# Kernel tuning notes

Measured on AMD Instinct MI355X. Metric: run time of the kernel, lower is better.

## Reference

```python
import jax, jax.numpy as jnp
import numpy as np

C, D, B, NS = 1000, 256, 16384, 200000
MOMENTUM = 0.1
TOPK = 5
EPS = 1e-12  # torch F.normalize default eps


def _cos_distance(a, b):
    # 0.5 * (1 - cos_sim) between rows of a [N,D] and rows of b [M,D]
    a = a / jnp.maximum(jnp.linalg.norm(a, axis=1, keepdims=True), EPS)
    b = b / jnp.maximum(jnp.linalg.norm(b, axis=1, keepdims=True), EPS)
    return 0.5 * (1.0 - jnp.einsum('nd,md->nm', a, b))


def setup_inputs() -> dict:
    key = jax.random.key(0)
    k1, k2, k3, k4 = jax.random.split(key, 4)
    return {
        'feature_source': jax.random.normal(k1, (B, D), jnp.float32),
        'center_mem': jax.random.normal(k2, (C, D), jnp.float32),
        'source_mem': jax.random.normal(k3, (NS, D), jnp.float32),
        'class2center': jnp.zeros((C, 2), jnp.float32),
        'interdist': jnp.zeros((C, C, 2), jnp.float32),
        'label_source': jax.random.randint(k4, (B,), 0, C, jnp.int32),
        'index_source': jnp.arange(B, dtype=jnp.int32),
    }


def reference(feature_source, center_mem, source_mem, class2center, interdist,
              label_source, index_source):
    # --- featuredistance2center: scatter-add per-class count and distance ---
    d1 = _cos_distance(feature_source, center_mem)            # [B, C]
    dist_at_label = jnp.take_along_axis(d1, label_source[:, None], axis=1)[:, 0]  # [B]
    class2center_new = class2center.at[label_source, 0].add(1.0)
    class2center_new = class2center_new.at[label_source, 1].add(dist_at_label)

    # --- update_center (labels_value=None): center += sum of features per class ---
    center_new = center_mem + jax.ops.segment_sum(feature_source, label_source,
                                                  num_segments=C)  # [C, D]

    # --- update_source: momentum scatter update of the source feature bank ---
    old = source_mem[index_source]                             # [B, D]
    source_mem_new = source_mem.at[index_source].set((1.0 - MOMENTUM) * old
                                                     + MOMENTUM * feature_source)

    # --- sourcefeature2differertcenter: topk-smallest distances, scatter-add ---
    d2 = _cos_distance(feature_source, center_new)             # [B, C]
    neg_vals, top_idx = jax.lax.top_k(-d2, TOPK)               # smallest distances
    top_dists = -neg_vals                                      # [B, TOPK]
    top1, top2 = top_idx[:, 0], top_idx[:, 1]
    inter = jnp.abs(top_dists[:, 0] - top_dists[:, 1])         # [B]
    interdist_new = interdist.at[top1, top2, 0].add(1.0)
    interdist_new = interdist_new.at[top1, top2, 1].add(inter)

    return (center_new, source_mem_new, class2center_new, interdist_new)
```

## Files before the change

### kernel.cpp

```cpp
#include <hip/hip_runtime.h>
#include <math.h>

#define Cc 1000
#define Cpad 1024
#define Dd 256
#define Bb 16384
#define NSs 200000
#define MOM 0.1f
#define EPSV 1e-12f
#define EPSC 0.10f

#define OUT_CENTER 0
#define OUT_SRC (Cc*Dd)
#define OUT_C2C (OUT_SRC + (size_t)NSs*Dd)
#define OUT_INTER (OUT_C2C + Cc*2)

#define SCR_SCORES 0
#define SCR_FB ((size_t)Bb * Cpad)
#define SCR_CB (SCR_FB + (size_t)Bb*Dd/2)

#define WS_CHAT 0
#define WS_INVF (Cc*Dd)

#define NEG_BIG (-3.4e38f)

typedef __bf16 bf16x8 __attribute__((ext_vector_type(8)));
typedef float  f32x4  __attribute__((ext_vector_type(4)));

__device__ __forceinline__ ushort f2bf(float f) {
    uint u = __float_as_uint(f);
    u += 0x7FFFu + ((u >> 16) & 1u);
    return (ushort)(u >> 16);
}

__device__ __forceinline__ void upd_top2(float& s1, int& i1, float& s2, int& i2,
                                         float s, int i) {
    if (s > s1 || (s == s1 && i < i1)) {
        s2 = s1; i2 = i1; s1 = s; i1 = i;
    } else if (s > s2 || (s == s2 && i < i2)) {
        s2 = s; i2 = i;
    }
}

__global__ void k_copy(const float4* __restrict__ interdist,
                       const float4* __restrict__ c2c,
                       const float4* __restrict__ cmem,
                       float4* __restrict__ out_inter,
                       float4* __restrict__ out_c2c,
                       float4* __restrict__ out_center) {
    int i = blockIdx.x * blockDim.x + threadIdx.x;
    const int n_inter = Cc * Cc * 2 / 4;
    const int n_c2c   = Cc * 2 / 4;
    const int n_cm    = Cc * Dd / 4;
    if (i < n_inter) {
        out_inter[i] = interdist[i];
    } else if (i < n_inter + n_c2c) {
        out_c2c[i - n_inter] = c2c[i - n_inter];
    } else if (i < n_inter + n_c2c + n_cm) {
        out_center[i - n_inter - n_c2c] = cmem[i - n_inter - n_c2c];
    }
}

__global__ void k_rows_a(const float* __restrict__ feat, const float* __restrict__ cmem,
                         const int* __restrict__ label,
                         float* __restrict__ out_center, float* __restrict__ out_c2c,
                         float* __restrict__ ws_invf, ushort* __restrict__ fb) {
    int wid  = threadIdx.x >> 6;
    int lane = threadIdx.x & 63;
    int row  = blockIdx.x * 4 + wid;
    if (row >= Bb) return;

    const float4 f4 = *(const float4*)(feat + (size_t)row * Dd + lane * 4);
    int lab = label[row];
    const float4 c4 = *(const float4*)(cmem + (size_t)lab * Dd + lane * 4);

    ushort4 h;
    h.x = f2bf(f4.x); h.y = f2bf(f4.y); h.z = f2bf(f4.z); h.w = f2bf(f4.w);
    *(ushort4*)(fb + (size_t)row * Dd + lane * 4) = h;

    float fs = f4.x*f4.x + f4.y*f4.y + f4.z*f4.z + f4.w*f4.w;
    float dt = f4.x*c4.x + f4.y*c4.y + f4.z*c4.z + f4.w*c4.w;
    float cs = c4.x*c4.x + c4.y*c4.y + c4.z*c4.z + c4.w*c4.w;
    #pragma unroll
    for (int off = 32; off; off >>= 1) {
        fs += __shfl_xor(fs, off);
        dt += __shfl_xor(dt, off);
        cs += __shfl_xor(cs, off);
    }
    float invf = 1.0f / fmaxf(sqrtf(fs), EPSV);
    if (lane == 0) {
        ws_invf[row] = invf;
        float invc = 1.0f / fmaxf(sqrtf(cs), EPSV);
        float d1 = 0.5f * (1.0f - dt * invf * invc);
        atomicAdd(out_c2c + lab * 2,     1.0f);
        atomicAdd(out_c2c + lab * 2 + 1, d1);
    }
    atomicAdd(out_center + (size_t)lab * Dd + lane * 4 + 0, f4.x);
    atomicAdd(out_center + (size_t)lab * Dd + lane * 4 + 1, f4.y);
    atomicAdd(out_center + (size_t)lab * Dd + lane * 4 + 2, f4.z);
    atomicAdd(out_center + (size_t)lab * Dd + lane * 4 + 3, f4.w);
}

__global__ void k_chat(const float* __restrict__ out_center, float* __restrict__ chat,
                       ushort* __restrict__ cb) {
    int c = blockIdx.x;
    int lane = threadIdx.x;
    if (c >= Cc) {
        ushort4 z; z.x = 0; z.y = 0; z.z = 0; z.w = 0;
        *(ushort4*)(cb + (size_t)c * Dd + lane * 4) = z;
        return;
    }
    float4 v = *(const float4*)(out_center + (size_t)c * Dd + lane * 4);
    float ss = v.x*v.x + v.y*v.y + v.z*v.z + v.w*v.w;
    #pragma unroll
    for (int off = 32; off; off >>= 1) ss += __shfl_xor(ss, off);
    float inv = 1.0f / fmaxf(sqrtf(ss), EPSV);
    float4 r; r.x = v.x*inv; r.y = v.y*inv; r.z = v.z*inv; r.w = v.w*inv;
    *(float4*)(chat + (size_t)c * Dd + lane * 4) = r;
    ushort4 h;
    h.x = f2bf(r.x); h.y = f2bf(r.y); h.z = f2bf(r.z); h.w = f2bf(r.w);
    *(ushort4*)(cb + (size_t)c * Dd + lane * 4) = h;
}

__global__ __launch_bounds__(256) void k_gemm(const ushort* __restrict__ fb,
                                              const ushort* __restrict__ cb,
                                              float* __restrict__ scores) {
    int wid  = threadIdx.x >> 6;
    int lane = threadIdx.x & 63;
    int rl = lane & 15;
    int kg = lane >> 4;
    int row0 = blockIdx.y * 64;
    int c0   = blockIdx.x * 256 + wid * 64;

    const ushort* fp = fb + (size_t)(row0 + rl) * Dd + kg * 8;
    const ushort* cp = cb + (size_t)(c0  + rl) * Dd + kg * 8;

    f32x4 acc[4][4];
    f32x4 z = {0.f, 0.f, 0.f, 0.f};
    #pragma unroll
    for (int mi = 0; mi < 4; mi++)
        #pragma unroll
        for (int ni = 0; ni < 4; ni++)
            acc[mi][ni] = z;

    #pragma unroll
    for (int ks = 0; ks < 8; ks++) {
        bf16x8 a[4], b[4];
        #pragma unroll
        for (int mi = 0; mi < 4; mi++)
            a[mi] = *(const bf16x8*)(fp + (size_t)mi * 16 * Dd + ks * 32);
        #pragma unroll
        for (int ni = 0; ni < 4; ni++)
            b[ni] = *(const bf16x8*)(cp + (size_t)ni * 16 * Dd + ks * 32);
        #pragma unroll
        for (int mi = 0; mi < 4; mi++)
            #pragma unroll
            for (int ni = 0; ni < 4; ni++)
                acc[mi][ni] = __builtin_amdgcn_mfma_f32_16x16x32_bf16(a[mi], b[ni], acc[mi][ni], 0, 0, 0);
    }

    #pragma unroll
    for (int mi = 0; mi < 4; mi++)
        #pragma unroll
        for (int ni = 0; ni < 4; ni++)
            #pragma unroll
            for (int r = 0; r < 4; r++)
                scores[(size_t)(row0 + mi*16 + kg*4 + r) * Cpad + (c0 + ni*16 + rl)] = acc[mi][ni][r];
}

__global__ __launch_bounds__(256) void k_sel(const float* __restrict__ scores,
                                             const float* __restrict__ feat,
                                             const float* __restrict__ chat,
                                             const float* __restrict__ ws_invf,
                                             float* __restrict__ out_inter) {
    __shared__ int cnt[4];
    __shared__ int clist[4][32];
    int wid  = threadIdx.x >> 6;
    int lane = threadIdx.x & 63;
    int row  = blockIdx.x * 4 + wid;
    if (lane == 0) cnt[wid] = 0;

    const float4* sp = (const float4*)(scores + (size_t)row * Cpad);
    float v[16];
    float s1 = NEG_BIG, s2 = NEG_BIG;
    int   i1 = 0x7fffffff, i2 = 0x7fffffff;
    #pragma unroll
    for (int j = 0; j < 4; j++) {
        float4 q = sp[j * 64 + lane];
        int cbase = j * 256 + lane * 4;
        v[j*4+0] = q.x; v[j*4+1] = q.y; v[j*4+2] = q.z; v[j*4+3] = q.w;
        if (cbase + 0 < Cc) upd_top2(s1, i1, s2, i2, q.x, cbase + 0);
        if (cbase + 1 < Cc) upd_top2(s1, i1, s2, i2, q.y, cbase + 1);
        if (cbase + 2 < Cc) upd_top2(s1, i1, s2, i2, q.z, cbase + 2);
        if (cbase + 3 < Cc) upd_top2(s1, i1, s2, i2, q.w, cbase + 3);
    }
    #pragma unroll
    for (int off = 1; off < 64; off <<= 1) {
        float ps1 = __shfl_xor(s1, off), ps2 = __shfl_xor(s2, off);
        int   pi1 = __shfl_xor(i1, off), pi2 = __shfl_xor(i2, off);
        upd_top2(s1, i1, s2, i2, ps1, pi1);
        upd_top2(s1, i1, s2, i2, ps2, pi2);
    }
    float thr = s2 - EPSC;
    #pragma unroll
    for (int j = 0; j < 16; j++) {
        int c = (j >> 2) * 256 + lane * 4 + (j & 3);
        if (v[j] >= thr && c < Cc) {
            int slot = atomicAdd(&cnt[wid], 1);
            if (slot < 32) clist[wid][slot] = c;
        }
    }
    __syncthreads();
    int n = cnt[wid]; if (n > 32) n = 32;

    const float4 f4 = *(const float4*)(feat + (size_t)row * Dd + lane * 4);
    float S1 = NEG_BIG, S2 = NEG_BIG;
    int   I1 = 0x7fffffff, I2 = 0x7fffffff;
    for (int k = 0; k < n; k++) {
        int c = clist[wid][k];
        const float4 c4 = *(const float4*)(chat + (size_t)c * Dd + lane * 4);
        float d = f4.x*c4.x + f4.y*c4.y + f4.z*c4.z + f4.w*c4.w;
        #pragma unroll
        for (int off = 32; off; off >>= 1) d += __shfl_xor(d, off);
        upd_top2(S1, I1, S2, I2, d, c);
    }
    if (lane == 0) {
        float inter = 0.5f * ws_invf[row] * (S1 - S2);
        size_t off2 = ((size_t)I1 * Cc + I2) * 2;
        atomicAdd(out_inter + off2,     1.0f);
        atomicAdd(out_inter + off2 + 1, inter);
    }
}

__global__ void k_srccopy(const float4* __restrict__ src, float4* __restrict__ dst, int n4) {
    int stride = gridDim.x * blockDim.x;
    for (int i = blockIdx.x * blockDim.x + threadIdx.x; i < n4; i += stride)
        dst[i] = src[i];
}

__global__ void k_rows_b(const float* __restrict__ feat, const float* __restrict__ smem,
                         const int* __restrict__ index, float* __restrict__ out_src) {
    int wid  = threadIdx.x >> 6;
    int lane = threadIdx.x & 63;
    int row  = blockIdx.x * 4 + wid;
    if (row >= Bb) return;
    int idx = index[row];
    const float4 f4 = *(const float4*)(feat + (size_t)row * Dd + lane * 4);
    const float4 o4 = *(const float4*)(smem + (size_t)idx * Dd + lane * 4);
    float4 r;
    r.x = (1.0f - MOM) * o4.x + MOM * f4.x;
    r.y = (1.0f - MOM) * o4.y + MOM * f4.y;
    r.z = (1.0f - MOM) * o4.z + MOM * f4.z;
    r.w = (1.0f - MOM) * o4.w + MOM * f4.w;
    *(float4*)(out_src + (size_t)idx * Dd + lane * 4) = r;
}

extern "C" void kernel_launch(void* const* d_in, const int* in_sizes, int n_in,
                              void* d_out, int out_size, void* d_ws, size_t ws_size,
                              hipStream_t stream) {
    const float* feat   = (const float*)d_in[0];
    const float* cmem   = (const float*)d_in[1];
    const float* smem   = (const float*)d_in[2];
    const float* c2c    = (const float*)d_in[3];
    const float* inter  = (const float*)d_in[4];
    const int*   label  = (const int*)d_in[5];
    const int*   index  = (const int*)d_in[6];

    float* out = (float*)d_out;
    float* out_center = out + OUT_CENTER;
    float* out_src    = out + OUT_SRC;
    float* out_c2c    = out + OUT_C2C;
    float* out_inter  = out + OUT_INTER;

    float* ws    = (float*)d_ws;
    float* chat  = ws + WS_CHAT;
    float* winvf = ws + WS_INVF;

    float*  scores = out_src + SCR_SCORES;
    ushort* fb     = (ushort*)(out_src + SCR_FB);
    ushort* cb     = (ushort*)(out_src + SCR_CB);

    {
        int total4 = Cc*Cc*2/4 + Cc*2/4 + Cc*Dd/4;
        int blocks = (total4 + 255) / 256;
        k_copy<<<blocks, 256, 0, stream>>>((const float4*)inter, (const float4*)c2c,
                                           (const float4*)cmem,
                                           (float4*)out_inter, (float4*)out_c2c,
                                           (float4*)out_center);
    }
    k_rows_a<<<Bb / 4, 256, 0, stream>>>(feat, cmem, label, out_center, out_c2c, winvf, fb);
    k_chat<<<Cpad, 64, 0, stream>>>(out_center, chat, cb);
    {
        dim3 grid(4, Bb / 64);
        k_gemm<<<grid, 256, 0, stream>>>(fb, cb, scores);
    }
    k_sel<<<Bb / 4, 256, 0, stream>>>(scores, feat, chat, winvf, out_inter);
    {
        int n4 = NSs * Dd / 4;
        k_srccopy<<<2048, 256, 0, stream>>>((const float4*)smem, (float4*)out_src, n4);
    }
    k_rows_b<<<Bb / 4, 256, 0, stream>>>(feat, smem, index, out_src);
}
```

Measured before the change: 295.7 us.

## Fuse top-2 selection into GEMM epilogue and merge source bank copy with momentum update

The GEMM epilogue now does a per-row top-2 reduction within each 64-column tile and writes only per-tile partials plus a short list of near-threshold candidates. This replaces writing the full 16384x1024 score matrix and reading it back in a separate selection kernel. The source bank copy and the momentum scatter are merged into one streaming pass that uses an index-to-row mark array, so each scattered row is no longer written twice. In exchange the GEMM takes extra register pressure, shuffles and global atomics. Candidates are capped per row, so unusually dense rows could drop entries.

```diff
diff --git a/kernel.cpp b/kernel.cpp
--- a/kernel.cpp
+++ b/kernel.cpp
@@ -9,20 +9,25 @@
 #define MOM 0.1f
 #define EPSV 1e-12f
 #define EPSC 0.10f
+#define CANDCAP 48
+#define LISTCAP 40
+#define NEG_BIG (-3.4e38f)
+#define IDX_BIG 0x7fffffff
 
 #define OUT_CENTER 0
 #define OUT_SRC (Cc*Dd)
 #define OUT_C2C (OUT_SRC + (size_t)NSs*Dd)
 #define OUT_INTER (OUT_C2C + Cc*2)
 
-#define SCR_SCORES 0
-#define SCR_FB ((size_t)Bb * Cpad)
-#define SCR_CB (SCR_FB + (size_t)Bb*Dd/2)
+#define SCR_FB 0
+#define SCR_CB 2097152
+#define SCR_PART 2228224
+#define SCR_CAND 3276800
+#define SCR_CNT 4849664
 
 #define WS_CHAT 0
-#define WS_INVF (Cc*Dd)
-
-#define NEG_BIG (-3.4e38f)
+#define WS_INVF 256000
+#define WS_MARK 272384
 
 typedef __bf16 bf16x8 __attribute__((ext_vector_type(8)));
 typedef float  f32x4  __attribute__((ext_vector_type(4)));
@@ -42,23 +47,39 @@
     }
 }
 
-__global__ void k_copy(const float4* __restrict__ interdist,
+#define N_INTER4 (Cc*Cc*2/4)
+#define N_C2C4   (Cc*2/4)
+#define N_CM4    (Cc*Dd/4)
+#define N_MARK4  (NSs/4)
+#define N_CNT4   (Bb/4)
+#define N_INIT4  (N_INTER4 + N_C2C4 + N_CM4 + N_MARK4 + N_CNT4)
+
+__global__ void k_init(const float4* __restrict__ interdist,
                        const float4* __restrict__ c2c,
                        const float4* __restrict__ cmem,
                        float4* __restrict__ out_inter,
                        float4* __restrict__ out_c2c,
-                       float4* __restrict__ out_center) {
+                       float4* __restrict__ out_center,
+                       int4* __restrict__ mark, int4* __restrict__ cnt) {
     int i = blockIdx.x * blockDim.x + threadIdx.x;
-    const int n_inter = Cc * Cc * 2 / 4;
-    const int n_c2c   = Cc * 2 / 4;
-    const int n_cm    = Cc * Dd / 4;
-    if (i < n_inter) {
+    if (i < N_INTER4) {
         out_inter[i] = interdist[i];
-    } else if (i < n_inter + n_c2c) {
-        out_c2c[i - n_inter] = c2c[i - n_inter];
-    } else if (i < n_inter + n_c2c + n_cm) {
-        out_center[i - n_inter - n_c2c] = cmem[i - n_inter - n_c2c];
-    }
+    } else if (i < N_INTER4 + N_C2C4) {
+        out_c2c[i - N_INTER4] = c2c[i - N_INTER4];
+    } else if (i < N_INTER4 + N_C2C4 + N_CM4) {
+        out_center[i - N_INTER4 - N_C2C4] = cmem[i - N_INTER4 - N_C2C4];
+    } else if (i < N_INTER4 + N_C2C4 + N_CM4 + N_MARK4) {
+        int4 m; m.x = -1; m.y = -1; m.z = -1; m.w = -1;
+        mark[i - N_INTER4 - N_C2C4 - N_CM4] = m;
+    } else if (i < N_INIT4) {
+        int4 z; z.x = 0; z.y = 0; z.z = 0; z.w = 0;
+        cnt[i - N_INTER4 - N_C2C4 - N_CM4 - N_MARK4] = z;
+    }
+}
+
+__global__ void k_scatter(const int* __restrict__ index, int* __restrict__ mark) {
+    int i = blockIdx.x * blockDim.x + threadIdx.x;
+    if (i < Bb) mark[index[i]] = i;
 }
 
 __global__ void k_rows_a(const float* __restrict__ feat, const float* __restrict__ cmem,
@@ -124,13 +145,16 @@
 
 __global__ __launch_bounds__(256) void k_gemm(const ushort* __restrict__ fb,
                                               const ushort* __restrict__ cb,
-                                              float* __restrict__ scores) {
+                                              float4* __restrict__ part,
+                                              float2* __restrict__ cand,
+                                              int* __restrict__ cnt) {
     int wid  = threadIdx.x >> 6;
     int lane = threadIdx.x & 63;
     int rl = lane & 15;
     int kg = lane >> 4;
     int row0 = blockIdx.y * 64;
     int c0   = blockIdx.x * 256 + wid * 64;
+    int tile = blockIdx.x * 4 + wid;
 
     const ushort* fp = fb + (size_t)(row0 + rl) * Dd + kg * 8;
     const ushort* cp = cb + (size_t)(c0  + rl) * Dd + kg * 8;
@@ -159,100 +183,131 @@
                 acc[mi][ni] = __builtin_amdgcn_mfma_f32_16x16x32_bf16(a[mi], b[ni], acc[mi][ni], 0, 0, 0);
     }
 
+    float S1[16], S2[16];
+    int   I1[16], I2[16];
+    #pragma unroll
+    for (int j = 0; j < 16; j++) { S1[j] = NEG_BIG; S2[j] = NEG_BIG; I1[j] = IDX_BIG; I2[j] = IDX_BIG; }
     #pragma unroll
     for (int mi = 0; mi < 4; mi++)
         #pragma unroll
-        for (int ni = 0; ni < 4; ni++)
+        for (int r = 0; r < 4; r++)
             #pragma unroll
-            for (int r = 0; r < 4; r++)
-                scores[(size_t)(row0 + mi*16 + kg*4 + r) * Cpad + (c0 + ni*16 + rl)] = acc[mi][ni][r];
-}
-
-__global__ __launch_bounds__(256) void k_sel(const float* __restrict__ scores,
+            for (int ni = 0; ni < 4; ni++) {
+                int col = c0 + ni * 16 + rl;
+                if (col < Cc)
+                    upd_top2(S1[mi*4+r], I1[mi*4+r], S2[mi*4+r], I2[mi*4+r], acc[mi][ni][r], col);
+            }
+    #pragma unroll
+    for (int off = 1; off < 16; off <<= 1)
+        #pragma unroll
+        for (int j = 0; j < 16; j++) {
+            float t1 = __shfl_xor(S1[j], off), t2 = __shfl_xor(S2[j], off);
+            int   u1 = __shfl_xor(I1[j], off), u2 = __shfl_xor(I2[j], off);
+            upd_top2(S1[j], I1[j], S2[j], I2[j], t1, u1);
+            upd_top2(S1[j], I1[j], S2[j], I2[j], t2, u2);
+        }
+    #pragma unroll
+    for (int mi = 0; mi < 4; mi++)
+        #pragma unroll
+        for (int r = 0; r < 4; r++)
+            #pragma unroll
+            for (int ni = 0; ni < 4; ni++) {
+                int col = c0 + ni * 16 + rl;
+                float v = acc[mi][ni][r];
+                int j = mi*4 + r;
+                if (col < Cc && v >= S2[j] - EPSC && col != I1[j] && col != I2[j]) {
+                    int row = row0 + mi * 16 + kg * 4 + r;
+                    int slot = atomicAdd(cnt + row, 1);
+                    if (slot < CANDCAP)
+                        cand[(size_t)row * CANDCAP + slot] = make_float2(v, __int_as_float(col));
+                }
+            }
+    #pragma unroll
+    for (int j = 0; j < 16; j++) {
+        if (rl == j) {
+            int row = row0 + (j >> 2) * 16 + kg * 4 + (j & 3);
+            part[(size_t)row * 16 + tile] =
+                make_float4(S1[j], S2[j], __int_as_float(I1[j]), __int_as_float(I2[j]));
+        }
+    }
+}
+
+__global__ __launch_bounds__(256) void k_fin(const float4* __restrict__ part,
+                                             const float2* __restrict__ cand,
+                                             const int* __restrict__ cnt,
                                              const float* __restrict__ feat,
                                              const float* __restrict__ chat,
                                              const float* __restrict__ ws_invf,
                                              float* __restrict__ out_inter) {
-    __shared__ int cnt[4];
-    __shared__ int clist[4][32];
+    __shared__ int lcnt[4];
+    __shared__ int lst[4][LISTCAP];
     int wid  = threadIdx.x >> 6;
     int lane = threadIdx.x & 63;
     int row  = blockIdx.x * 4 + wid;
-    if (lane == 0) cnt[wid] = 0;
-
-    const float4* sp = (const float4*)(scores + (size_t)row * Cpad);
-    float v[16];
-    float s1 = NEG_BIG, s2 = NEG_BIG;
-    int   i1 = 0x7fffffff, i2 = 0x7fffffff;
-    #pragma unroll
-    for (int j = 0; j < 4; j++) {
-        float4 q = sp[j * 64 + lane];
-        int cbase = j * 256 + lane * 4;
-        v[j*4+0] = q.x; v[j*4+1] = q.y; v[j*4+2] = q.z; v[j*4+3] = q.w;
-        if (cbase + 0 < Cc) upd_top2(s1, i1, s2, i2, q.x, cbase + 0);
-        if (cbase + 1 < Cc) upd_top2(s1, i1, s2, i2, q.y, cbase + 1);
-        if (cbase + 2 < Cc) upd_top2(s1, i1, s2, i2, q.z, cbase + 2);
-        if (cbase + 3 < Cc) upd_top2(s1, i1, s2, i2, q.w, cbase + 3);
-    }
+    if (lane == 0) lcnt[wid] = 0;
+
+    float4 p;
+    if (lane < 16) p = part[(size_t)row * 16 + lane];
+    else p = make_float4(NEG_BIG, NEG_BIG, __int_as_float(IDX_BIG), __int_as_float(IDX_BIG));
+
+    float s1 = p.x, s2 = p.y;
+    int   i1 = __float_as_int(p.z), i2 = __float_as_int(p.w);
     #pragma unroll
     for (int off = 1; off < 64; off <<= 1) {
-        float ps1 = __shfl_xor(s1, off), ps2 = __shfl_xor(s2, off);
-        int   pi1 = __shfl_xor(i1, off), pi2 = __shfl_xor(i2, off);
-        upd_top2(s1, i1, s2, i2, ps1, pi1);
-        upd_top2(s1, i1, s2, i2, ps2, pi2);
+        float t1 = __shfl_xor(s1, off), t2 = __shfl_xor(s2, off);
+        int   u1 = __shfl_xor(i1, off), u2 = __shfl_xor(i2, off);
+        upd_top2(s1, i1, s2, i2, t1, u1);
+        upd_top2(s1, i1, s2, i2, t2, u2);
     }
     float thr = s2 - EPSC;
-    #pragma unroll
-    for (int j = 0; j < 16; j++) {
-        int c = (j >> 2) * 256 + lane * 4 + (j & 3);
-        if (v[j] >= thr && c < Cc) {
-            int slot = atomicAdd(&cnt[wid], 1);
-            if (slot < 32) clist[wid][slot] = c;
-        }
+    if (lane < 16) {
+        if (p.x >= thr) { int s = atomicAdd(&lcnt[wid], 1); if (s < LISTCAP) lst[wid][s] = __float_as_int(p.z); }
+        if (p.y >= thr) { int s = atomicAdd(&lcnt[wid], 1); if (s < LISTCAP) lst[wid][s] = __float_as_int(p.w); }
+    }
+    int n = cnt[row]; if (n > CANDCAP) n = CANDCAP;
+    if (lane < n) {
+        float2 cv = cand[(size_t)row * CANDCAP + lane];
+        if (cv.x >= thr) { int s = atomicAdd(&lcnt[wid], 1); if (s < LISTCAP) lst[wid][s] = __float_as_int(cv.y); }
     }
     __syncthreads();
-    int n = cnt[wid]; if (n > 32) n = 32;
+    int m = lcnt[wid]; if (m > LISTCAP) m = LISTCAP;
 
     const float4 f4 = *(const float4*)(feat + (size_t)row * Dd + lane * 4);
-    float S1 = NEG_BIG, S2 = NEG_BIG;
-    int   I1 = 0x7fffffff, I2 = 0x7fffffff;
-    for (int k = 0; k < n; k++) {
-        int c = clist[wid][k];
-        const float4 c4 = *(const float4*)(chat + (size_t)c * Dd + lane * 4);
+    float F1 = NEG_BIG, F2 = NEG_BIG;
+    int   J1 = IDX_BIG, J2 = IDX_BIG;
+    for (int k = 0; k < m; k++) {
+        int col = lst[wid][k];
+        const float4 c4 = *(const float4*)(chat + (size_t)col * Dd + lane * 4);
         float d = f4.x*c4.x + f4.y*c4.y + f4.z*c4.z + f4.w*c4.w;
         #pragma unroll
         for (int off = 32; off; off >>= 1) d += __shfl_xor(d, off);
-        upd_top2(S1, I1, S2, I2, d, c);
+        upd_top2(F1, J1, F2, J2, d, col);
     }
     if (lane == 0) {
-        float inter = 0.5f * ws_invf[row] * (S1 - S2);
-        size_t off2 = ((size_t)I1 * Cc + I2) * 2;
+        float inter = 0.5f * ws_invf[row] * (F1 - F2);
+        size_t off2 = ((size_t)J1 * Cc + J2) * 2;
         atomicAdd(out_inter + off2,     1.0f);
         atomicAdd(out_inter + off2 + 1, inter);
     }
 }
 
-__global__ void k_srccopy(const float4* __restrict__ src, float4* __restrict__ dst, int n4) {
+__global__ void k_src(const float4* __restrict__ src, const float4* __restrict__ feat,
+                      const int* __restrict__ mark, float4* __restrict__ dst) {
+    const int n4 = NSs * Dd / 4;
     int stride = gridDim.x * blockDim.x;
-    for (int i = blockIdx.x * blockDim.x + threadIdx.x; i < n4; i += stride)
-        dst[i] = src[i];
-}
-
-__global__ void k_rows_b(const float* __restrict__ feat, const float* __restrict__ smem,
-                         const int* __restrict__ index, float* __restrict__ out_src) {
-    int wid  = threadIdx.x >> 6;
-    int lane = threadIdx.x & 63;
-    int row  = blockIdx.x * 4 + wid;
-    if (row >= Bb) return;
-    int idx = index[row];
-    const float4 f4 = *(const float4*)(feat + (size_t)row * Dd + lane * 4);
-    const float4 o4 = *(const float4*)(smem + (size_t)idx * Dd + lane * 4);
-    float4 r;
-    r.x = (1.0f - MOM) * o4.x + MOM * f4.x;
-    r.y = (1.0f - MOM) * o4.y + MOM * f4.y;
-    r.z = (1.0f - MOM) * o4.z + MOM * f4.z;
-    r.w = (1.0f - MOM) * o4.w + MOM * f4.w;
-    *(float4*)(out_src + (size_t)idx * Dd + lane * 4) = r;
+    for (int e = blockIdx.x * blockDim.x + threadIdx.x; e < n4; e += stride) {
+        int row = e >> 6;
+        int m = mark[row];
+        float4 v = src[e];
+        if (m >= 0) {
+            float4 f = feat[(size_t)m * 64 + (e & 63)];
+            v.x = (1.0f - MOM) * v.x + MOM * f.x;
+            v.y = (1.0f - MOM) * v.y + MOM * f.y;
+            v.z = (1.0f - MOM) * v.z + MOM * f.z;
+            v.w = (1.0f - MOM) * v.w + MOM * f.w;
+        }
+        dst[e] = v;
+    }
 }
 
 extern "C" void kernel_launch(void* const* d_in, const int* in_sizes, int n_in,
@@ -275,29 +330,26 @@
     float* ws    = (float*)d_ws;
     float* chat  = ws + WS_CHAT;
     float* winvf = ws + WS_INVF;
-
-    float*  scores = out_src + SCR_SCORES;
-    ushort* fb     = (ushort*)(out_src + SCR_FB);
-    ushort* cb     = (ushort*)(out_src + SCR_CB);
-
-    {
-        int total4 = Cc*Cc*2/4 + Cc*2/4 + Cc*Dd/4;
-        int blocks = (total4 + 255) / 256;
-        k_copy<<<blocks, 256, 0, stream>>>((const float4*)inter, (const float4*)c2c,
-                                           (const float4*)cmem,
-                                           (float4*)out_inter, (float4*)out_c2c,
-                                           (float4*)out_center);
-    }
+    int*   mark  = (int*)(ws + WS_MARK);
+
+    ushort* fb    = (ushort*)(out_src + SCR_FB);
+    ushort* cb    = (ushort*)(out_src + SCR_CB);
+    float4* part  = (float4*)(out_src + SCR_PART);
+    float2* cand  = (float2*)(out_src + SCR_CAND);
+    int*    cnt   = (int*)(out_src + SCR_CNT);
+
+    k_init<<<(N_INIT4 + 255) / 256, 256, 0, stream>>>(
+        (const float4*)inter, (const float4*)c2c, (const float4*)cmem,
+        (float4*)out_inter, (float4*)out_c2c, (float4*)out_center,
+        (int4*)mark, (int4*)cnt);
+    k_scatter<<<Bb / 256, 256, 0, stream>>>(index, mark);
     k_rows_a<<<Bb / 4, 256, 0, stream>>>(feat, cmem, label, out_center, out_c2c, winvf, fb);
     k_chat<<<Cpad, 64, 0, stream>>>(out_center, chat, cb);
     {
         dim3 grid(4, Bb / 64);
-        k_gemm<<<grid, 256, 0, stream>>>(fb, cb, scores);
-    }
-    k_sel<<<Bb / 4, 256, 0, stream>>>(scores, feat, chat, winvf, out_inter);
-    {
-        int n4 = NSs * Dd / 4;
-        k_srccopy<<<2048, 256, 0, stream>>>((const float4*)smem, (float4*)out_src, n4);
-    }
-    k_rows_b<<<Bb / 4, 256, 0, stream>>>(feat, smem, index, out_src);
-}
+        k_gemm<<<grid, 256, 0, stream>>>(fb, cb, part, cand, cnt);
+    }
+    k_fin<<<Bb / 4, 256, 0, stream>>>(part, cand, cnt, feat, chat, winvf, out_inter);
+    k_src<<<4096, 256, 0, stream>>>((const float4*)smem, (const float4*)feat, mark,
+                                    (float4*)out_src);
+}
```

Measured after the change: 516.5 us. +74.7%, slower.

## Stage GEMM tiles in LDS and fuse source-bank momentum update into copy

Applied to the files above, without the earlier changes.

The bf16 MFMA GEMM now loads 128x128 tiles of features and centers into swizzled LDS with global_load_lds, then reads MFMA fragments from LDS. Previously each wave loaded its own fragments straight from global memory, so this cuts redundant global traffic. The source-bank copy and the separate row-scatter kernel are merged into one pass, using a row-to-batch mark array built by new init and scatter kernels. This drops the second read and write of the updated rows, at the cost of an extra mark lookup per element and two tiny kernels. If index contains duplicates, the winning entry now depends on which scatter write lands last.

```diff
diff --git a/kernel.cpp b/kernel.cpp
--- a/kernel.cpp
+++ b/kernel.cpp
@@ -9,6 +9,8 @@
 #define MOM 0.1f
 #define EPSV 1e-12f
 #define EPSC 0.10f
+#define NEG_BIG (-3.4e38f)
+#define IDX_BIG 0x7fffffff
 
 #define OUT_CENTER 0
 #define OUT_SRC (Cc*Dd)
@@ -20,9 +22,8 @@
 #define SCR_CB (SCR_FB + (size_t)Bb*Dd/2)
 
 #define WS_CHAT 0
-#define WS_INVF (Cc*Dd)
-
-#define NEG_BIG (-3.4e38f)
+#define WS_INVF 256000
+#define WS_MARK 272384
 
 typedef __bf16 bf16x8 __attribute__((ext_vector_type(8)));
 typedef float  f32x4  __attribute__((ext_vector_type(4)));
@@ -31,6 +32,12 @@
     uint u = __float_as_uint(f);
     u += 0x7FFFu + ((u >> 16) & 1u);
     return (ushort)(u >> 16);
+}
+
+__device__ __forceinline__ void gload16(const void* g, void* l) {
+    __builtin_amdgcn_global_load_lds(
+        (const __attribute__((address_space(1))) void*)g,
+        (__attribute__((address_space(3))) void*)l, 16, 0, 0);
 }
 
 __device__ __forceinline__ void upd_top2(float& s1, int& i1, float& s2, int& i2,
@@ -42,23 +49,35 @@
     }
 }
 
-__global__ void k_copy(const float4* __restrict__ interdist,
+#define N_INTER4 (Cc*Cc*2/4)
+#define N_C2C4   (Cc*2/4)
+#define N_CM4    (Cc*Dd/4)
+#define N_MARK4  (NSs/4)
+#define N_INIT4  (N_INTER4 + N_C2C4 + N_CM4 + N_MARK4)
+
+__global__ void k_init(const float4* __restrict__ interdist,
                        const float4* __restrict__ c2c,
                        const float4* __restrict__ cmem,
                        float4* __restrict__ out_inter,
                        float4* __restrict__ out_c2c,
-                       float4* __restrict__ out_center) {
+                       float4* __restrict__ out_center,
+                       int4* __restrict__ mark) {
     int i = blockIdx.x * blockDim.x + threadIdx.x;
-    const int n_inter = Cc * Cc * 2 / 4;
-    const int n_c2c   = Cc * 2 / 4;
-    const int n_cm    = Cc * Dd / 4;
-    if (i < n_inter) {
+    if (i < N_INTER4) {
         out_inter[i] = interdist[i];
-    } else if (i < n_inter + n_c2c) {
-        out_c2c[i - n_inter] = c2c[i - n_inter];
-    } else if (i < n_inter + n_c2c + n_cm) {
-        out_center[i - n_inter - n_c2c] = cmem[i - n_inter - n_c2c];
-    }
+    } else if (i < N_INTER4 + N_C2C4) {
+        out_c2c[i - N_INTER4] = c2c[i - N_INTER4];
+    } else if (i < N_INTER4 + N_C2C4 + N_CM4) {
+        out_center[i - N_INTER4 - N_C2C4] = cmem[i - N_INTER4 - N_C2C4];
+    } else if (i < N_INIT4) {
+        int4 m; m.x = -1; m.y = -1; m.z = -1; m.w = -1;
+        mark[i - N_INTER4 - N_C2C4 - N_CM4] = m;
+    }
+}
+
+__global__ void k_scatter(const int* __restrict__ index, int* __restrict__ mark) {
+    int i = blockIdx.x * blockDim.x + threadIdx.x;
+    if (i < Bb) mark[index[i]] = i;
 }
 
 __global__ void k_rows_a(const float* __restrict__ feat, const float* __restrict__ cmem,
@@ -122,18 +141,23 @@
     *(ushort4*)(cb + (size_t)c * Dd + lane * 4) = h;
 }
 
-__global__ __launch_bounds__(256) void k_gemm(const ushort* __restrict__ fb,
-                                              const ushort* __restrict__ cb,
-                                              float* __restrict__ scores) {
-    int wid  = threadIdx.x >> 6;
-    int lane = threadIdx.x & 63;
+__global__ __launch_bounds__(256, 2) void k_gemm(const ushort* __restrict__ fb,
+                                                 const ushort* __restrict__ cb,
+                                                 float* __restrict__ scores) {
+    __shared__ __align__(16) char Asb[128 * 128];
+    __shared__ __align__(16) char Bsb[128 * 128];
+
+    int tid  = threadIdx.x;
+    int wid  = tid >> 6;
+    int lane = tid & 63;
     int rl = lane & 15;
     int kg = lane >> 4;
-    int row0 = blockIdx.y * 64;
-    int c0   = blockIdx.x * 256 + wid * 64;
-
-    const ushort* fp = fb + (size_t)(row0 + rl) * Dd + kg * 8;
-    const ushort* cp = cb + (size_t)(c0  + rl) * Dd + kg * 8;
+    int wr = wid >> 1;
+    int wc = wid & 1;
+    int row0 = blockIdx.y * 128;
+    int c0   = blockIdx.x * 128;
+
+    int realb = ((lane & 7) ^ (lane >> 3)) << 4;
 
     f32x4 acc[4][4];
     f32x4 z = {0.f, 0.f, 0.f, 0.f};
@@ -143,29 +167,65 @@
         for (int ni = 0; ni < 4; ni++)
             acc[mi][ni] = z;
 
-    #pragma unroll
-    for (int ks = 0; ks < 8; ks++) {
-        bf16x8 a[4], b[4];
-        #pragma unroll
-        for (int mi = 0; mi < 4; mi++)
-            a[mi] = *(const bf16x8*)(fp + (size_t)mi * 16 * Dd + ks * 32);
-        #pragma unroll
-        for (int ni = 0; ni < 4; ni++)
-            b[ni] = *(const bf16x8*)(cp + (size_t)ni * 16 * Dd + ks * 32);
+    for (int t = 0; t < 4; t++) {
+        #pragma unroll
+        for (int i = 0; i < 4; i++) {
+            int rloc = wid * 32 + i * 8;
+            int grow = row0 + rloc + (lane >> 3);
+            gload16((const char*)(fb + (size_t)grow * Dd) + t * 128 + realb,
+                    Asb + rloc * 128);
+        }
+        #pragma unroll
+        for (int i = 0; i < 4; i++) {
+            int rloc = wid * 32 + i * 8;
+            int gcol = c0 + rloc + (lane >> 3);
+            gload16((const char*)(cb + (size_t)gcol * Dd) + t * 128 + realb,
+                    Bsb + rloc * 128);
+        }
+        asm volatile("s_waitcnt vmcnt(0)" ::: "memory");
+        __syncthreads();
+
+        bf16x8 a[4][2], b[4][2];
         #pragma unroll
         for (int mi = 0; mi < 4; mi++)
             #pragma unroll
-            for (int ni = 0; ni < 4; ni++)
-                acc[mi][ni] = __builtin_amdgcn_mfma_f32_16x16x32_bf16(a[mi], b[ni], acc[mi][ni], 0, 0, 0);
-    }
-
-    #pragma unroll
-    for (int mi = 0; mi < 4; mi++)
+            for (int ks = 0; ks < 2; ks++) {
+                int r = wr * 64 + mi * 16 + rl;
+                int off = r * 128 + ((ks * 64 + kg * 16) ^ ((r & 7) << 4));
+                a[mi][ks] = *(const bf16x8*)(Asb + off);
+            }
         #pragma unroll
         for (int ni = 0; ni < 4; ni++)
             #pragma unroll
-            for (int r = 0; r < 4; r++)
-                scores[(size_t)(row0 + mi*16 + kg*4 + r) * Cpad + (c0 + ni*16 + rl)] = acc[mi][ni][r];
+            for (int ks = 0; ks < 2; ks++) {
+                int r = wc * 64 + ni * 16 + rl;
+                int off = r * 128 + ((ks * 64 + kg * 16) ^ ((r & 7) << 4));
+                b[ni][ks] = *(const bf16x8*)(Bsb + off);
+            }
+
+        #pragma unroll
+        for (int ks = 0; ks < 2; ks++)
+            #pragma unroll
+            for (int mi = 0; mi < 4; mi++)
+                #pragma unroll
+                for (int ni = 0; ni < 4; ni++)
+                    acc[mi][ni] = __builtin_amdgcn_mfma_f32_16x16x32_bf16(
+                        a[mi][ks], b[ni][ks], acc[mi][ni], 0, 0, 0);
+
+        __syncthreads();
+    }
+
+    #pragma unroll
+    for (int mi = 0; mi < 4; mi++) {
+        int row = row0 + wr * 64 + mi * 16 + kg * 4;
+        #pragma unroll
+        for (int ni = 0; ni < 4; ni++) {
+            int col = c0 + wc * 64 + ni * 16 + rl;
+            #pragma unroll
+            for (int rr = 0; rr < 4; rr++)
+                scores[(size_t)(row + rr) * Cpad + col] = acc[mi][ni][rr];
+        }
+    }
 }
 
 __global__ __launch_bounds__(256) void k_sel(const float* __restrict__ scores,
@@ -183,7 +243,7 @@
     const float4* sp = (const float4*)(scores + (size_t)row * Cpad);
     float v[16];
     float s1 = NEG_BIG, s2 = NEG_BIG;
-    int   i1 = 0x7fffffff, i2 = 0x7fffffff;
+    int   i1 = IDX_BIG, i2 = IDX_BIG;
     #pragma unroll
     for (int j = 0; j < 4; j++) {
         float4 q = sp[j * 64 + lane];
@@ -215,7 +275,7 @@
 
     const float4 f4 = *(const float4*)(feat + (size_t)row * Dd + lane * 4);
     float S1 = NEG_BIG, S2 = NEG_BIG;
-    int   I1 = 0x7fffffff, I2 = 0x7fffffff;
+    int   I1 = IDX_BIG, I2 = IDX_BIG;
     for (int k = 0; k < n; k++) {
         int c = clist[wid][k];
         const float4 c4 = *(const float4*)(chat + (size_t)c * Dd + lane * 4);
@@ -232,27 +292,23 @@
     }
 }
 
-__global__ void k_srccopy(const float4* __restrict__ src, float4* __restrict__ dst, int n4) {
+__global__ void k_src(const float4* __restrict__ src, const float4* __restrict__ feat,
+                      const int* __restrict__ mark, float4* __restrict__ dst) {
+    const int n4 = NSs * Dd / 4;
     int stride = gridDim.x * blockDim.x;
-    for (int i = blockIdx.x * blockDim.x + threadIdx.x; i < n4; i += stride)
-        dst[i] = src[i];
-}
-
-__global__ void k_rows_b(const float* __restrict__ feat, const float* __restrict__ smem,
-                         const int* __restrict__ index, float* __restrict__ out_src) {
-    int wid  = threadIdx.x >> 6;
-    int lane = threadIdx.x & 63;
-    int row  = blockIdx.x * 4 + wid;
-    if (row >= Bb) return;
-    int idx = index[row];
-    const float4 f4 = *(const float4*)(feat + (size_t)row * Dd + lane * 4);
-    const float4 o4 = *(const float4*)(smem + (size_t)idx * Dd + lane * 4);
-    float4 r;
-    r.x = (1.0f - MOM) * o4.x + MOM * f4.x;
-    r.y = (1.0f - MOM) * o4.y + MOM * f4.y;
-    r.z = (1.0f - MOM) * o4.z + MOM * f4.z;
-    r.w = (1.0f - MOM) * o4.w + MOM * f4.w;
-    *(float4*)(out_src + (size_t)idx * Dd + lane * 4) = r;
+    for (int e = blockIdx.x * blockDim.x + threadIdx.x; e < n4; e += stride) {
+        int row = e >> 6;
+        int m = mark[row];
+        float4 v = src[e];
+        if (m >= 0) {
+            float4 f = feat[(size_t)m * 64 + (e & 63)];
+            v.x = (1.0f - MOM) * v.x + MOM * f.x;
+            v.y = (1.0f - MOM) * v.y + MOM * f.y;
+            v.z = (1.0f - MOM) * v.z + MOM * f.z;
+            v.w = (1.0f - MOM) * v.w + MOM * f.w;
+        }
+        dst[e] = v;
+    }
 }
 
 extern "C" void kernel_launch(void* const* d_in, const int* in_sizes, int n_in,
@@ -275,29 +331,24 @@
     float* ws    = (float*)d_ws;
     float* chat  = ws + WS_CHAT;
     float* winvf = ws + WS_INVF;
+    int*   mark  = (int*)(ws + WS_MARK);
 
     float*  scores = out_src + SCR_SCORES;
     ushort* fb     = (ushort*)(out_src + SCR_FB);
     ushort* cb     = (ushort*)(out_src + SCR_CB);
 
-    {
-        int total4 = Cc*Cc*2/4 + Cc*2/4 + Cc*Dd/4;
-        int blocks = (total4 + 255) / 256;
-        k_copy<<<blocks, 256, 0, stream>>>((const float4*)inter, (const float4*)c2c,
-                                           (const float4*)cmem,
-                                           (float4*)out_inter, (float4*)out_c2c,
-                                           (float4*)out_center);
-    }
+    k_init<<<(N_INIT4 + 255) / 256, 256, 0, stream>>>(
+        (const float4*)inter, (const float4*)c2c, (const float4*)cmem,
+        (float4*)out_inter, (float4*)out_c2c, (float4*)out_center,
+        (int4*)mark);
+    k_scatter<<<Bb / 256, 256, 0, stream>>>(index, mark);
     k_rows_a<<<Bb / 4, 256, 0, stream>>>(feat, cmem, label, out_center, out_c2c, winvf, fb);
     k_chat<<<Cpad, 64, 0, stream>>>(out_center, chat, cb);
     {
-        dim3 grid(4, Bb / 64);
+        dim3 grid(Cpad / 128, Bb / 128);
         k_gemm<<<grid, 256, 0, stream>>>(fb, cb, scores);
     }
     k_sel<<<Bb / 4, 256, 0, stream>>>(scores, feat, chat, winvf, out_inter);
-    {
-        int n4 = NSs * Dd / 4;
-        k_srccopy<<<2048, 256, 0, stream>>>((const float4*)smem, (float4*)out_src, n4);
-    }
-    k_rows_b<<<Bb / 4, 256, 0, stream>>>(feat, smem, index, out_src);
-}
+    k_src<<<4096, 256, 0, stream>>>((const float4*)smem, (const float4*)feat, mark,
+                                    (float4*)out_src);
+}
```

Result: faster. 269.5 us (-8.8%).
